# Performance work log

Measured on AMD Instinct MI355X. Metric: run time of the kernel, lower is better.

The kernel has to match this reference:

```python
import jax, jax.numpy as jnp
import numpy as np

C = 256
CQK = C // 8  # 32

def setup_inputs() -> dict:
    key = jax.random.key(0)
    ks = jax.random.split(key, 8)
    B, H, W = 8, 64, 64
    x = jax.random.normal(ks[0], (B, C, H, W), dtype=jnp.float32)
    y = jax.random.normal(ks[1], (B, C, H, W), dtype=jnp.float32)
    s = 1.0 / np.sqrt(C)
    Wq = jax.random.normal(ks[2], (CQK, C), dtype=jnp.float32) * s
    bq = jnp.zeros((CQK,), dtype=jnp.float32)
    Wk = jax.random.normal(ks[3], (CQK, C), dtype=jnp.float32) * s
    bk = jnp.zeros((CQK,), dtype=jnp.float32)
    Wv = jax.random.normal(ks[4], (C, C), dtype=jnp.float32) * s
    bv = jnp.zeros((C,), dtype=jnp.float32)
    return {"x": x, "y": y, "Wq": Wq, "bq": bq, "Wk": Wk, "bk": bk, "Wv": Wv, "bv": bv}

def reference(x, y, Wq, bq, Wk, bk, Wv, bv):
    B, Cc, H, W = x.shape
    HW = H * W
    xf = x.reshape(B, Cc, HW)  # [B,C,HW]
    yf = y.reshape(B, Cc, HW)
    # 1x1 convs == per-pixel linear projections
    Q = jnp.einsum('oc,bcn->bno', Wq, xf) + bq          # [B,HW,CQK]
    K = jnp.einsum('oc,bcn->bon', Wk, yf) + bk[:, None]  # [B,CQK,HW]
    V = jnp.einsum('oc,bcn->bon', Wv, yf) + bv[:, None]  # [B,C,HW]
    attn = jax.nn.softmax(jnp.einsum('bnd,bdm->bnm', Q, K), axis=-1)  # [B,HW,HW]
    out = jnp.einsum('bcm,bnm->bcn', V, attn)  # V @ attn^T -> [B,C,HW]
    return out.reshape(B, Cc, H, W)
```

## Files before the change

kernel.cpp:

```cpp
#include <hip/hip_runtime.h>

typedef unsigned short u16;
typedef _Float16 f16;
typedef __attribute__((ext_vector_type(8))) short v8s;
typedef __attribute__((ext_vector_type(4))) short v4s;
typedef __attribute__((ext_vector_type(8))) f16   v8h;
typedef __attribute__((ext_vector_type(4))) float v4f;
typedef __attribute__((ext_vector_type(16))) float v16f;
typedef __attribute__((ext_vector_type(4))) unsigned v4u;

#define NB   8
#define NC   256
#define DQK  32
#define NPIX 4096

__device__ __forceinline__ u16 f2bf(float f) {
  unsigned u = __builtin_bit_cast(unsigned, f);
  u += 0x7FFFu + ((u >> 16) & 1u);
  return (u16)(u >> 16);
}
__device__ __forceinline__ u16 f2h(float f) {
  return __builtin_bit_cast(u16, (f16)f);
}
__device__ __forceinline__ unsigned cvt_pk_bf16(float lo, float hi) {
  unsigned r;
  asm("v_cvt_pk_bf16_f32 %0, %1, %2" : "=v"(r) : "v"(lo), "v"(hi));
  return r;
}
__device__ __forceinline__ float fast_exp2(float x) {
  float r;
  asm("v_exp_f32 %0, %1" : "=v"(r) : "v"(x));
  return r;
}

__global__ __launch_bounds__(256)
void convert_w(const float* __restrict__ Wq, const float* __restrict__ Wk,
               const float* __restrict__ Wv,
               u16* __restrict__ Whq, u16* __restrict__ Whk, u16* __restrict__ Whv) {
  int i = blockIdx.x * 256 + threadIdx.x;
  if (i < 8192)       Whq[i]         = f2h(Wq[i]);
  else if (i < 16384) Whk[i - 8192]  = f2h(Wk[i - 8192]);
  else                Whv[i - 16384] = f2h(Wv[i - 16384]);
}

__global__ __launch_bounds__(256)
void proj_fused(const float* __restrict__ x, const float* __restrict__ y,
                const u16* __restrict__ Whq, const float* __restrict__ bq,
                const u16* __restrict__ Whk, const float* __restrict__ bk,
                const u16* __restrict__ Whv, const float* __restrict__ bv,
                u16* __restrict__ Qb, u16* __restrict__ Kb, u16* __restrict__ Vt) {
  __shared__ u16 Tx[64][66], Ty[64][66];

  const int tid = threadIdx.x, w = tid >> 6, lane = tid & 63;
  const int lr = lane & 15, quad = lane >> 4;
  const int nl = lane;
  const int b = blockIdx.x & 7;
  const int n0 = (blockIdx.x >> 3) * 64;
  const int n = n0 + w * 16 + lr;
  const size_t bn = ((size_t)b << 12) + n;
  const int col = w * 16 + lr;

  v4f aq[2], ak[2], av[16];
#pragma unroll
  for (int ot = 0; ot < 2; ++ot) { aq[ot] = (v4f){0.f,0.f,0.f,0.f}; ak[ot] = (v4f){0.f,0.f,0.f,0.f}; }
#pragma unroll
  for (int vt = 0; vt < 16; ++vt) av[vt] = (v4f){0.f,0.f,0.f,0.f};

#pragma unroll 1
  for (int cs = 0; cs < 4; ++cs) {
    if (cs) __syncthreads();
    const float* __restrict__ xs = x + ((size_t)b << 20) + (size_t)(cs * 64) * NPIX + n0;
    const float* __restrict__ ys = y + ((size_t)b << 20) + (size_t)(cs * 64) * NPIX + n0;
#pragma unroll
    for (int i = 0; i < 16; ++i) {
      int c = w * 16 + i;
      Tx[c][nl] = f2h(xs[(size_t)c * NPIX + nl]);
      Ty[c][nl] = f2h(ys[(size_t)c * NPIX + nl]);
    }
    __syncthreads();

    v8s tx0, tx1, ty0, ty1;
#pragma unroll
    for (int j = 0; j < 8; ++j) {
      tx0[j] = (short)Tx[quad * 8 + j][col];
      tx1[j] = (short)Tx[32 + quad * 8 + j][col];
      ty0[j] = (short)Ty[quad * 8 + j][col];
      ty1[j] = (short)Ty[32 + quad * 8 + j][col];
    }
    const v8h xb0 = __builtin_bit_cast(v8h, tx0);
    const v8h xb1 = __builtin_bit_cast(v8h, tx1);
    const v8h yb0 = __builtin_bit_cast(v8h, ty0);
    const v8h yb1 = __builtin_bit_cast(v8h, ty1);

#pragma unroll
    for (int ot = 0; ot < 2; ++ot) {
      const u16* wqp = Whq + (ot * 16 + lr) * 256 + cs * 64 + quad * 8;
      const u16* wkp = Whk + (ot * 16 + lr) * 256 + cs * 64 + quad * 8;
      aq[ot] = __builtin_amdgcn_mfma_f32_16x16x32_f16(*(const v8h*)(wqp),      xb0, aq[ot], 0, 0, 0);
      aq[ot] = __builtin_amdgcn_mfma_f32_16x16x32_f16(*(const v8h*)(wqp + 32), xb1, aq[ot], 0, 0, 0);
      ak[ot] = __builtin_amdgcn_mfma_f32_16x16x32_f16(*(const v8h*)(wkp),      yb0, ak[ot], 0, 0, 0);
      ak[ot] = __builtin_amdgcn_mfma_f32_16x16x32_f16(*(const v8h*)(wkp + 32), yb1, ak[ot], 0, 0, 0);
    }
#pragma unroll
    for (int vt = 0; vt < 16; ++vt) {
      const u16* wvp = Whv + (vt * 16 + lr) * 256 + cs * 64 + quad * 8;
      av[vt] = __builtin_amdgcn_mfma_f32_16x16x32_f16(*(const v8h*)(wvp),      yb0, av[vt], 0, 0, 0);
      av[vt] = __builtin_amdgcn_mfma_f32_16x16x32_f16(*(const v8h*)(wvp + 32), yb1, av[vt], 0, 0, 0);
    }
  }

#pragma unroll
  for (int ot = 0; ot < 2; ++ot) {
    v4f bqv = *(const v4f*)(bq + ot * 16 + quad * 4);
    v4f bkv = *(const v4f*)(bk + ot * 16 + quad * 4);
    v4s q4, k4;
#pragma unroll
    for (int r = 0; r < 4; ++r) {
      q4[r] = (short)f2h(aq[ot][r] + bqv[r]);
      k4[r] = (short)f2h(ak[ot][r] + bkv[r]);
    }
    *(v4s*)(Qb + bn * DQK + ot * 16 + quad * 4) = q4;
    *(v4s*)(Kb + bn * DQK + ot * 16 + quad * 4) = k4;
  }

#pragma unroll
  for (int vt = 0; vt < 16; ++vt) {
#pragma unroll
    for (int r = 0; r < 4; ++r) {
      int o = vt * 16 + quad * 4 + r;
      size_t off = ((((size_t)b * 64 + (n >> 6)) * 32 + (o >> 5) * 4 + ((n >> 4) & 3)) * 64
                    + ((n >> 3) & 1) * 32 + (o & 31)) * 8 + (n & 7);
      Vt[off] = f2bf(av[vt][r] + bv[o]);
    }
  }
}

#define L2E  1.44269504f
#define SHFT -48.0f

#define PACK_TILE(S, PBLO, PBHI)                                              \
  {                                                                           \
    float e0  = fast_exp2(fmaf(S[0],  L2E, SHFT));                            \
    float e1  = fast_exp2(fmaf(S[1],  L2E, SHFT));                            \
    float e2  = fast_exp2(fmaf(S[2],  L2E, SHFT));                            \
    float e3  = fast_exp2(fmaf(S[3],  L2E, SHFT));                            \
    float e4  = fast_exp2(fmaf(S[4],  L2E, SHFT));                            \
    float e5  = fast_exp2(fmaf(S[5],  L2E, SHFT));                            \
    float e6  = fast_exp2(fmaf(S[6],  L2E, SHFT));                            \
    float e7  = fast_exp2(fmaf(S[7],  L2E, SHFT));                            \
    float e8  = fast_exp2(fmaf(S[8],  L2E, SHFT));                            \
    float e9  = fast_exp2(fmaf(S[9],  L2E, SHFT));                            \
    float e10 = fast_exp2(fmaf(S[10], L2E, SHFT));                            \
    float e11 = fast_exp2(fmaf(S[11], L2E, SHFT));                            \
    float e12 = fast_exp2(fmaf(S[12], L2E, SHFT));                            \
    float e13 = fast_exp2(fmaf(S[13], L2E, SHFT));                            \
    float e14 = fast_exp2(fmaf(S[14], L2E, SHFT));                            \
    float e15 = fast_exp2(fmaf(S[15], L2E, SHFT));                            \
    lsum += (((e0 + e1) + (e2 + e3)) + ((e4 + e5) + (e6 + e7)))               \
          + (((e8 + e9) + (e10 + e11)) + ((e12 + e13) + (e14 + e15)));        \
    unsigned u00 = cvt_pk_bf16(e0,  e1),  u01 = cvt_pk_bf16(e2,  e3);         \
    unsigned u10 = cvt_pk_bf16(e4,  e5),  u11 = cvt_pk_bf16(e6,  e7);         \
    unsigned u20 = cvt_pk_bf16(e8,  e9),  u21 = cvt_pk_bf16(e10, e11);        \
    unsigned u30 = cvt_pk_bf16(e12, e13), u31 = cvt_pk_bf16(e14, e15);        \
    asm("v_permlane32_swap_b32 %0, %1" : "+v"(u00), "+v"(u10));               \
    asm("v_permlane32_swap_b32 %0, %1" : "+v"(u01), "+v"(u11));               \
    asm("v_permlane32_swap_b32 %0, %1" : "+v"(u20), "+v"(u30));               \
    asm("v_permlane32_swap_b32 %0, %1" : "+v"(u21), "+v"(u31));               \
    PBLO = __builtin_bit_cast(v8s, (v4u){u00, u01, u10, u11});                \
    PBHI = __builtin_bit_cast(v8s, (v4u){u20, u21, u30, u31});                \
  }

__global__ __launch_bounds__(512, 2)
void attn_kernel(const u16* __restrict__ Qb, const u16* __restrict__ Kb,
                 const u16* __restrict__ Vt, float* __restrict__ out) {
  __shared__ __attribute__((aligned(16))) u16 Vb[4][32][64][8];
  __shared__ float Ls2[4][32];

  const int tid  = threadIdx.x;
  const int w    = tid >> 6;
  const int lane = tid & 63;
  const int l31  = lane & 31;
  const int wq   = w & 3;
  const int g    = w >> 2;
  const int bufbase = g * 2;

  const int b  = blockIdx.x & 7;
  const int q0 = (blockIdx.x >> 3) << 7;
  const int qw = q0 + wq * 32;

  const int h = lane >> 5;
  const u16* Qp = Qb + ((size_t)b * NPIX + qw + l31) * DQK + h * 8;
  const v8h qf0 = *(const v8h*)(Qp);
  const v8h qf1 = *(const v8h*)(Qp + 16);

  const u16* Kp = Kb + ((size_t)b * NPIX + l31) * DQK + h * 8 + (size_t)g * 32 * 2048;

  const u16* Vg = Vt + ((size_t)b << 20) + (size_t)lane * 8 + (size_t)g * 32 * 16384;

  v16f acc[8];
#pragma unroll
  for (int i = 0; i < 8; ++i) acc[i] = (v16f){};
  float lsum = 0.f;
  const v16f vz = (v16f){};

#pragma unroll
  for (int j = 0; j < 8; ++j) {
    const int f = wq * 8 + j;
    __builtin_amdgcn_global_load_lds(
        (const __attribute__((address_space(1))) unsigned*)(Vg + (size_t)f * 512),
        (__attribute__((address_space(3))) unsigned*)(&Vb[bufbase][f][0][0]), 16, 0, 0);
  }
  v8h kc0 = *(const v8h*)(Kp);
  v8h kc1 = *(const v8h*)(Kp + 16);
  v8h kc2 = *(const v8h*)(Kp + 1024);
  v8h kc3 = *(const v8h*)(Kp + 1040);
  v8h kn0 = kc0, kn1 = kc1, kn2 = kc2, kn3 = kc3;

  v8s pB0, pB1, pB2, pB3;
  {
    v16f sA = __builtin_amdgcn_mfma_f32_32x32x16_f16(kc0, qf0, vz, 0, 0, 0);
    sA = __builtin_amdgcn_mfma_f32_32x32x16_f16(kc1, qf1, sA, 0, 0, 0);
    v16f sB = __builtin_amdgcn_mfma_f32_32x32x16_f16(kc2, qf0, vz, 0, 0, 0);
    sB = __builtin_amdgcn_mfma_f32_32x32x16_f16(kc3, qf1, sB, 0, 0, 0);
    PACK_TILE(sA, pB0, pB1);
    PACK_TILE(sB, pB2, pB3);
  }
  {
    const u16* kp1 = Kp + 2048;
    kc0 = *(const v8h*)(kp1);
    kc1 = *(const v8h*)(kp1 + 16);
    kc2 = *(const v8h*)(kp1 + 1024);
    kc3 = *(const v8h*)(kp1 + 1040);
  }

#pragma unroll 1
  for (int it = 0; it < 32; ++it) {
    const int pp = it & 1;
    __builtin_amdgcn_sched_barrier(0);
    if (it < 31) {
      asm volatile("s_waitcnt vmcnt(4)" ::: "memory");
    } else {
      asm volatile("s_waitcnt vmcnt(0)" ::: "memory");
    }
    __builtin_amdgcn_s_barrier();
    __builtin_amdgcn_sched_barrier(0);

    if (it < 31) {
#pragma unroll
      for (int j = 0; j < 8; ++j) {
        const int f = wq * 8 + j;
        __builtin_amdgcn_global_load_lds(
            (const __attribute__((address_space(1))) unsigned*)(Vg + ((size_t)(it + 1) * 32 + f) * 512),
            (__attribute__((address_space(3))) unsigned*)(&Vb[bufbase + (pp ^ 1)][f][0][0]), 16, 0, 0);
      }
    }

    __builtin_amdgcn_s_setprio(1);
#pragma unroll
    for (int ct = 0; ct < 8; ++ct) {
      v8s vf0 = *(const v8s*)(&Vb[bufbase + pp][ct * 4 + 0][lane][0]);
      v8s vf1 = *(const v8s*)(&Vb[bufbase + pp][ct * 4 + 1][lane][0]);
      v8s vf2 = *(const v8s*)(&Vb[bufbase + pp][ct * 4 + 2][lane][0]);
      v8s vf3 = *(const v8s*)(&Vb[bufbase + pp][ct * 4 + 3][lane][0]);
      acc[ct] = __builtin_amdgcn_mfma_f32_32x32x16_bf16(vf0, pB0, acc[ct], 0, 0, 0);
      acc[ct] = __builtin_amdgcn_mfma_f32_32x32x16_bf16(vf1, pB1, acc[ct], 0, 0, 0);
      acc[ct] = __builtin_amdgcn_mfma_f32_32x32x16_bf16(vf2, pB2, acc[ct], 0, 0, 0);
      acc[ct] = __builtin_amdgcn_mfma_f32_32x32x16_bf16(vf3, pB3, acc[ct], 0, 0, 0);
    }
    __builtin_amdgcn_s_setprio(0);

    if (it < 31) {
      v16f sA = __builtin_amdgcn_mfma_f32_32x32x16_f16(kc0, qf0, vz, 0, 0, 0);
      sA = __builtin_amdgcn_mfma_f32_32x32x16_f16(kc1, qf1, sA, 0, 0, 0);
      v16f sB = __builtin_amdgcn_mfma_f32_32x32x16_f16(kc2, qf0, vz, 0, 0, 0);
      sB = __builtin_amdgcn_mfma_f32_32x32x16_f16(kc3, qf1, sB, 0, 0, 0);
      if (it < 30) {
        const u16* kp2 = Kp + (size_t)(it + 2) * 2048;
        kn0 = *(const v8h*)(kp2);
        kn1 = *(const v8h*)(kp2 + 16);
        kn2 = *(const v8h*)(kp2 + 1024);
        kn3 = *(const v8h*)(kp2 + 1040);
      }
      PACK_TILE(sA, pB0, pB1);
      PACK_TILE(sB, pB2, pB3);
      kc0 = kn0; kc1 = kn1; kc2 = kn2; kc3 = kn3;
    }
  }

  lsum += __shfl_xor(lsum, 32);

  __syncthreads();
  float* Cb = (float*)&Vb[0][0][0][0];
  if (w >= 4) {
    const int w4 = w - 4;
#pragma unroll
    for (int ct = 0; ct < 8; ++ct)
#pragma unroll
      for (int k = 0; k < 4; ++k) {
        v4f c = {acc[ct][k * 4 + 0], acc[ct][k * 4 + 1],
                 acc[ct][k * 4 + 2], acc[ct][k * 4 + 3]};
        *(v4f*)(Cb + (((w4 * 32 + ct * 4 + k) * 64 + lane) << 2)) = c;
      }
    if (lane < 32) Ls2[w4][l31] = lsum;
  }
  __syncthreads();
  if (w < 4) {
    const float linv = 1.0f / (lsum + Ls2[w][l31]);
#pragma unroll
    for (int ct = 0; ct < 8; ++ct)
#pragma unroll
      for (int k = 0; k < 4; ++k) {
        v4f c = *(const v4f*)(Cb + (((w * 32 + ct * 4 + k) * 64 + lane) << 2));
        acc[ct][k * 4 + 0] += c[0]; acc[ct][k * 4 + 1] += c[1];
        acc[ct][k * 4 + 2] += c[2]; acc[ct][k * 4 + 3] += c[3];
      }

    float* op = out + (size_t)b * NC * NPIX + q0 + wq * 32 + l31;
#pragma unroll
    for (int ct = 0; ct < 8; ++ct)
#pragma unroll
      for (int r = 0; r < 16; ++r) {
        const int ch = ct * 32 + (r & 3) + ((r >> 2) << 3) + (h << 2);
        op[(size_t)ch * NPIX] = acc[ct][r] * linv;
      }
  }
}

extern "C" void kernel_launch(void* const* d_in, const int* in_sizes, int n_in,
                              void* d_out, int out_size, void* d_ws, size_t ws_size,
                              hipStream_t stream) {
  const float* x  = (const float*)d_in[0];
  const float* y  = (const float*)d_in[1];
  const float* Wq = (const float*)d_in[2];
  const float* bq = (const float*)d_in[3];
  const float* Wk = (const float*)d_in[4];
  const float* bk = (const float*)d_in[5];
  const float* Wv = (const float*)d_in[6];
  const float* bv = (const float*)d_in[7];
  float* out = (float*)d_out;

  u16* Qb  = (u16*)d_ws;
  u16* Kb  = Qb + (size_t)NB * NPIX * DQK;
  u16* Vt  = Kb + (size_t)NB * NPIX * DQK;
  u16* Whq = Vt + (size_t)NB * NC * NPIX;
  u16* Whk = Whq + 32 * 256;
  u16* Whv = Whk + 32 * 256;

  hipLaunchKernelGGL(convert_w, dim3(320), dim3(256), 0, stream, Wq, Wk, Wv, Whq, Whk, Whv);
  hipLaunchKernelGGL(proj_fused, dim3(512), dim3(256), 0, stream,
                     x, y, Whq, bq, Whk, bk, Whv, bv, Qb, Kb, Vt);
  hipLaunchKernelGGL(attn_kernel, dim3(256), dim3(512), 0, stream, Qb, Kb, Vt, out);
}
```

Measured before the change: 237.0 us.

## Fuse weight conversion, projections and attention into one cooperative kernel

Merges the three kernels into one cooperative launch, with grid-wide syncs separating weight conversion, the Q/K/V projection and attention. This removes two launch gaps. The projection now handles 128 pixels per 512-thread block, register-prefetches the next channel slab and writes the transposed tile to LDS with vector stores. The attention loop is unrolled by two with ping-pong P registers, and the next V stage is issued right after the barrier. Grid syncs add cost and require all 256 blocks to be co-resident.

```diff
diff --git a/kernel.cpp b/kernel.cpp
--- a/kernel.cpp
+++ b/kernel.cpp
@@ -1,4 +1,7 @@
 #include <hip/hip_runtime.h>
+#include <hip/hip_cooperative_groups.h>
+
+namespace cg = cooperative_groups;
 
 typedef unsigned short u16;
 typedef _Float16 f16;
@@ -31,108 +34,6 @@
   float r;
   asm("v_exp_f32 %0, %1" : "=v"(r) : "v"(x));
   return r;
-}
-
-__global__ __launch_bounds__(256)
-void convert_w(const float* __restrict__ Wq, const float* __restrict__ Wk,
-               const float* __restrict__ Wv,
-               u16* __restrict__ Whq, u16* __restrict__ Whk, u16* __restrict__ Whv) {
-  int i = blockIdx.x * 256 + threadIdx.x;
-  if (i < 8192)       Whq[i]         = f2h(Wq[i]);
-  else if (i < 16384) Whk[i - 8192]  = f2h(Wk[i - 8192]);
-  else                Whv[i - 16384] = f2h(Wv[i - 16384]);
-}
-
-__global__ __launch_bounds__(256)
-void proj_fused(const float* __restrict__ x, const float* __restrict__ y,
-                const u16* __restrict__ Whq, const float* __restrict__ bq,
-                const u16* __restrict__ Whk, const float* __restrict__ bk,
-                const u16* __restrict__ Whv, const float* __restrict__ bv,
-                u16* __restrict__ Qb, u16* __restrict__ Kb, u16* __restrict__ Vt) {
-  __shared__ u16 Tx[64][66], Ty[64][66];
-
-  const int tid = threadIdx.x, w = tid >> 6, lane = tid & 63;
-  const int lr = lane & 15, quad = lane >> 4;
-  const int nl = lane;
-  const int b = blockIdx.x & 7;
-  const int n0 = (blockIdx.x >> 3) * 64;
-  const int n = n0 + w * 16 + lr;
-  const size_t bn = ((size_t)b << 12) + n;
-  const int col = w * 16 + lr;
-
-  v4f aq[2], ak[2], av[16];
-#pragma unroll
-  for (int ot = 0; ot < 2; ++ot) { aq[ot] = (v4f){0.f,0.f,0.f,0.f}; ak[ot] = (v4f){0.f,0.f,0.f,0.f}; }
-#pragma unroll
-  for (int vt = 0; vt < 16; ++vt) av[vt] = (v4f){0.f,0.f,0.f,0.f};
-
-#pragma unroll 1
-  for (int cs = 0; cs < 4; ++cs) {
-    if (cs) __syncthreads();
-    const float* __restrict__ xs = x + ((size_t)b << 20) + (size_t)(cs * 64) * NPIX + n0;
-    const float* __restrict__ ys = y + ((size_t)b << 20) + (size_t)(cs * 64) * NPIX + n0;
-#pragma unroll
-    for (int i = 0; i < 16; ++i) {
-      int c = w * 16 + i;
-      Tx[c][nl] = f2h(xs[(size_t)c * NPIX + nl]);
-      Ty[c][nl] = f2h(ys[(size_t)c * NPIX + nl]);
-    }
-    __syncthreads();
-
-    v8s tx0, tx1, ty0, ty1;
-#pragma unroll
-    for (int j = 0; j < 8; ++j) {
-      tx0[j] = (short)Tx[quad * 8 + j][col];
-      tx1[j] = (short)Tx[32 + quad * 8 + j][col];
-      ty0[j] = (short)Ty[quad * 8 + j][col];
-      ty1[j] = (short)Ty[32 + quad * 8 + j][col];
-    }
-    const v8h xb0 = __builtin_bit_cast(v8h, tx0);
-    const v8h xb1 = __builtin_bit_cast(v8h, tx1);
-    const v8h yb0 = __builtin_bit_cast(v8h, ty0);
-    const v8h yb1 = __builtin_bit_cast(v8h, ty1);
-
-#pragma unroll
-    for (int ot = 0; ot < 2; ++ot) {
-      const u16* wqp = Whq + (ot * 16 + lr) * 256 + cs * 64 + quad * 8;
-      const u16* wkp = Whk + (ot * 16 + lr) * 256 + cs * 64 + quad * 8;
-      aq[ot] = __builtin_amdgcn_mfma_f32_16x16x32_f16(*(const v8h*)(wqp),      xb0, aq[ot], 0, 0, 0);
-      aq[ot] = __builtin_amdgcn_mfma_f32_16x16x32_f16(*(const v8h*)(wqp + 32), xb1, aq[ot], 0, 0, 0);
-      ak[ot] = __builtin_amdgcn_mfma_f32_16x16x32_f16(*(const v8h*)(wkp),      yb0, ak[ot], 0, 0, 0);
-      ak[ot] = __builtin_amdgcn_mfma_f32_16x16x32_f16(*(const v8h*)(wkp + 32), yb1, ak[ot], 0, 0, 0);
-    }
-#pragma unroll
-    for (int vt = 0; vt < 16; ++vt) {
-      const u16* wvp = Whv + (vt * 16 + lr) * 256 + cs * 64 + quad * 8;
-      av[vt] = __builtin_amdgcn_mfma_f32_16x16x32_f16(*(const v8h*)(wvp),      yb0, av[vt], 0, 0, 0);
-      av[vt] = __builtin_amdgcn_mfma_f32_16x16x32_f16(*(const v8h*)(wvp + 32), yb1, av[vt], 0, 0, 0);
-    }
-  }
-
-#pragma unroll
-  for (int ot = 0; ot < 2; ++ot) {
-    v4f bqv = *(const v4f*)(bq + ot * 16 + quad * 4);
-    v4f bkv = *(const v4f*)(bk + ot * 16 + quad * 4);
-    v4s q4, k4;
-#pragma unroll
-    for (int r = 0; r < 4; ++r) {
-      q4[r] = (short)f2h(aq[ot][r] + bqv[r]);
-      k4[r] = (short)f2h(ak[ot][r] + bkv[r]);
-    }
-    *(v4s*)(Qb + bn * DQK + ot * 16 + quad * 4) = q4;
-    *(v4s*)(Kb + bn * DQK + ot * 16 + quad * 4) = k4;
-  }
-
-#pragma unroll
-  for (int vt = 0; vt < 16; ++vt) {
-#pragma unroll
-    for (int r = 0; r < 4; ++r) {
-      int o = vt * 16 + quad * 4 + r;
-      size_t off = ((((size_t)b * 64 + (n >> 6)) * 32 + (o >> 5) * 4 + ((n >> 4) & 3)) * 64
-                    + ((n >> 3) & 1) * 32 + (o & 31)) * 8 + (n & 7);
-      Vt[off] = f2bf(av[vt][r] + bv[o]);
-    }
-  }
 }
 
 #define L2E  1.44269504f
@@ -170,159 +71,263 @@
     PBHI = __builtin_bit_cast(v8s, (v4u){u20, u21, u30, u31});                \
   }
 
+#define STAGE(IT, BUF)                                                        \
+  {                                                                           \
+    _Pragma("unroll")                                                         \
+    for (int j = 0; j < 8; ++j) {                                             \
+      const int f = wq * 8 + j;                                               \
+      __builtin_amdgcn_global_load_lds(                                       \
+          (const __attribute__((address_space(1))) unsigned*)(Vg + ((size_t)(IT) * 32 + f) * 512), \
+          (__attribute__((address_space(3))) unsigned*)(&SB[BUF][f][0][0]), 16, 0, 0); \
+    }                                                                         \
+  }
+
+#define ASTEP(I, PP, PI0, PI1, PI2, PI3, PO0, PO1, PO2, PO3)                  \
+  {                                                                           \
+    __builtin_amdgcn_sched_barrier(0);                                        \
+    if ((I) < 31) { asm volatile("s_waitcnt vmcnt(4)" ::: "memory"); }        \
+    else          { asm volatile("s_waitcnt vmcnt(0)" ::: "memory"); }        \
+    __builtin_amdgcn_s_barrier();                                             \
+    __builtin_amdgcn_sched_barrier(0);                                        \
+    if ((I) < 31) {                                                           \
+      STAGE((I) + 1, bufbase + ((PP) ^ 1));                                   \
+      v16f sA = __builtin_amdgcn_mfma_f32_32x32x16_f16(kc0, qf0, vz, 0, 0, 0);\
+      sA = __builtin_amdgcn_mfma_f32_32x32x16_f16(kc1, qf1, sA, 0, 0, 0);     \
+      PACK_TILE(sA, PO0, PO1);                                                \
+      v16f sB = __builtin_amdgcn_mfma_f32_32x32x16_f16(kc2, qf0, vz, 0, 0, 0);\
+      sB = __builtin_amdgcn_mfma_f32_32x32x16_f16(kc3, qf1, sB, 0, 0, 0);     \
+      PACK_TILE(sB, PO2, PO3);                                                \
+    }                                                                         \
+    if ((I) < 30) {   \
+      const u16* kp2 = Kp + (size_t)((I) + 2) * 2048;                         \
+      kc0 = *(const v8h*)(kp2);                                               \
+      kc1 = *(const v8h*)(kp2 + 16);                                          \
+      kc2 = *(const v8h*)(kp2 + 1024);                                        \
+      kc3 = *(const v8h*)(kp2 + 1040);                                        \
+    }                                                                         \
+    __builtin_amdgcn_s_setprio(1);                                            \
+    _Pragma("unroll")                                                         \
+    for (int ct = 0; ct < 8; ++ct) {                                          \
+      v8s vf0 = *(const v8s*)(&SB[bufbase + (PP)][ct * 4 + 0][lane][0]);      \
+      v8s vf1 = *(const v8s*)(&SB[bufbase + (PP)][ct * 4 + 1][lane][0]);      \
+      v8s vf2 = *(const v8s*)(&SB[bufbase + (PP)][ct * 4 + 2][lane][0]);      \
+      v8s vf3 = *(const v8s*)(&SB[bufbase + (PP)][ct * 4 + 3][lane][0]);      \
+      acc[ct] = __builtin_amdgcn_mfma_f32_32x32x16_bf16(vf0, PI0, acc[ct], 0, 0, 0); \
+      acc[ct] = __builtin_amdgcn_mfma_f32_32x32x16_bf16(vf1, PI1, acc[ct], 0, 0, 0); \
+      acc[ct] = __builtin_amdgcn_mfma_f32_32x32x16_bf16(vf2, PI2, acc[ct], 0, 0, 0); \
+      acc[ct] = __builtin_amdgcn_mfma_f32_32x32x16_bf16(vf3, PI3, acc[ct], 0, 0, 0); \
+    }                                                                         \
+    __builtin_amdgcn_s_setprio(0);                                            \
+  }
+
 __global__ __launch_bounds__(512, 2)
-void attn_kernel(const u16* __restrict__ Qb, const u16* __restrict__ Kb,
-                 const u16* __restrict__ Vt, float* __restrict__ out) {
-  __shared__ __attribute__((aligned(16))) u16 Vb[4][32][64][8];
+void fused_all(const float* __restrict__ x, const float* __restrict__ y,
+               const float* __restrict__ Wq, const float* __restrict__ bq,
+               const float* __restrict__ Wk, const float* __restrict__ bk,
+               const float* __restrict__ Wv, const float* __restrict__ bv,
+               u16* __restrict__ Qb, u16* __restrict__ Kb, u16* __restrict__ Vt,
+               u16* __restrict__ Whq, u16* __restrict__ Whk, u16* __restrict__ Whv,
+               float* __restrict__ out) {
+  __shared__ __attribute__((aligned(16))) u16 SB[4][32][64][8];
   __shared__ float Ls2[4][32];
 
   const int tid  = threadIdx.x;
   const int w    = tid >> 6;
   const int lane = tid & 63;
-  const int l31  = lane & 31;
-  const int wq   = w & 3;
-  const int g    = w >> 2;
-  const int bufbase = g * 2;
-
-  const int b  = blockIdx.x & 7;
-  const int q0 = (blockIdx.x >> 3) << 7;
-  const int qw = q0 + wq * 32;
-
-  const int h = lane >> 5;
-  const u16* Qp = Qb + ((size_t)b * NPIX + qw + l31) * DQK + h * 8;
-  const v8h qf0 = *(const v8h*)(Qp);
-  const v8h qf1 = *(const v8h*)(Qp + 16);
-
-  const u16* Kp = Kb + ((size_t)b * NPIX + l31) * DQK + h * 8 + (size_t)g * 32 * 2048;
-
-  const u16* Vg = Vt + ((size_t)b << 20) + (size_t)lane * 8 + (size_t)g * 32 * 16384;
-
-  v16f acc[8];
-#pragma unroll
-  for (int i = 0; i < 8; ++i) acc[i] = (v16f){};
-  float lsum = 0.f;
-  const v16f vz = (v16f){};
-
-#pragma unroll
-  for (int j = 0; j < 8; ++j) {
-    const int f = wq * 8 + j;
-    __builtin_amdgcn_global_load_lds(
-        (const __attribute__((address_space(1))) unsigned*)(Vg + (size_t)f * 512),
-        (__attribute__((address_space(3))) unsigned*)(&Vb[bufbase][f][0][0]), 16, 0, 0);
-  }
-  v8h kc0 = *(const v8h*)(Kp);
-  v8h kc1 = *(const v8h*)(Kp + 16);
-  v8h kc2 = *(const v8h*)(Kp + 1024);
-  v8h kc3 = *(const v8h*)(Kp + 1040);
-  v8h kn0 = kc0, kn1 = kc1, kn2 = kc2, kn3 = kc3;
-
-  v8s pB0, pB1, pB2, pB3;
+  const int lr   = lane & 15;
+  const int quad = lane >> 4;
+  const int b    = blockIdx.x & 7;
+  const int n0   = (blockIdx.x >> 3) * 128;
+
   {
-    v16f sA = __builtin_amdgcn_mfma_f32_32x32x16_f16(kc0, qf0, vz, 0, 0, 0);
-    sA = __builtin_amdgcn_mfma_f32_32x32x16_f16(kc1, qf1, sA, 0, 0, 0);
-    v16f sB = __builtin_amdgcn_mfma_f32_32x32x16_f16(kc2, qf0, vz, 0, 0, 0);
-    sB = __builtin_amdgcn_mfma_f32_32x32x16_f16(kc3, qf1, sB, 0, 0, 0);
-    PACK_TILE(sA, pB0, pB1);
-    PACK_TILE(sB, pB2, pB3);
-  }
+    int i = blockIdx.x * 512 + tid;
+    if (i < 8192)       Whq[i]         = f2h(Wq[i]);
+    else if (i < 16384) Whk[i - 8192]  = f2h(Wk[i - 8192]);
+    else if (i < 81920) Whv[i - 16384] = f2h(Wv[i - 16384]);
+  }
+  __threadfence();
+  cg::this_grid().sync();
+
   {
-    const u16* kp1 = Kp + 2048;
-    kc0 = *(const v8h*)(kp1);
-    kc1 = *(const v8h*)(kp1 + 16);
-    kc2 = *(const v8h*)(kp1 + 1024);
-    kc3 = *(const v8h*)(kp1 + 1040);
-  }
+    u16 (*Tx)[88] = reinterpret_cast<u16 (*)[88]>(&SB[0][0][0][0]);
+    u16 (*Ty)[88] = Tx + 128;
+
+    const int col = w * 16 + lr;
+    const int n = n0 + col;
+    const size_t bn = ((size_t)b << 12) + n;
+    const int srow  = (w >> 2) * 64 + lane;
+    const int scol0 = (w & 3) * 16;
+    const float* __restrict__ xs = x + ((size_t)b << 20) + n0 + srow;
+    const float* __restrict__ ys = y + ((size_t)b << 20) + n0 + srow;
+
+    v4f aq[2], ak[2], av[16];
+#pragma unroll
+    for (int ot = 0; ot < 2; ++ot) { aq[ot] = (v4f){0.f,0.f,0.f,0.f}; ak[ot] = (v4f){0.f,0.f,0.f,0.f}; }
+#pragma unroll
+    for (int vt = 0; vt < 16; ++vt) av[vt] = (v4f){0.f,0.f,0.f,0.f};
+
+    float xv[16], yv[16];
+#pragma unroll
+    for (int i = 0; i < 16; ++i) {
+      xv[i] = xs[(size_t)(scol0 + i) * NPIX];
+      yv[i] = ys[(size_t)(scol0 + i) * NPIX];
+    }
 
 #pragma unroll 1
-  for (int it = 0; it < 32; ++it) {
-    const int pp = it & 1;
-    __builtin_amdgcn_sched_barrier(0);
-    if (it < 31) {
-      asm volatile("s_waitcnt vmcnt(4)" ::: "memory");
-    } else {
-      asm volatile("s_waitcnt vmcnt(0)" ::: "memory");
-    }
-    __builtin_amdgcn_s_barrier();
-    __builtin_amdgcn_sched_barrier(0);
-
-    if (it < 31) {
-#pragma unroll
-      for (int j = 0; j < 8; ++j) {
-        const int f = wq * 8 + j;
-        __builtin_amdgcn_global_load_lds(
-            (const __attribute__((address_space(1))) unsigned*)(Vg + ((size_t)(it + 1) * 32 + f) * 512),
-            (__attribute__((address_space(3))) unsigned*)(&Vb[bufbase + (pp ^ 1)][f][0][0]), 16, 0, 0);
-      }
-    }
-
-    __builtin_amdgcn_s_setprio(1);
-#pragma unroll
-    for (int ct = 0; ct < 8; ++ct) {
-      v8s vf0 = *(const v8s*)(&Vb[bufbase + pp][ct * 4 + 0][lane][0]);
-      v8s vf1 = *(const v8s*)(&Vb[bufbase + pp][ct * 4 + 1][lane][0]);
-      v8s vf2 = *(const v8s*)(&Vb[bufbase + pp][ct * 4 + 2][lane][0]);
-      v8s vf3 = *(const v8s*)(&Vb[bufbase + pp][ct * 4 + 3][lane][0]);
-      acc[ct] = __builtin_amdgcn_mfma_f32_32x32x16_bf16(vf0, pB0, acc[ct], 0, 0, 0);
-      acc[ct] = __builtin_amdgcn_mfma_f32_32x32x16_bf16(vf1, pB1, acc[ct], 0, 0, 0);
-      acc[ct] = __builtin_amdgcn_mfma_f32_32x32x16_bf16(vf2, pB2, acc[ct], 0, 0, 0);
-      acc[ct] = __builtin_amdgcn_mfma_f32_32x32x16_bf16(vf3, pB3, acc[ct], 0, 0, 0);
-    }
-    __builtin_amdgcn_s_setprio(0);
-
-    if (it < 31) {
-      v16f sA = __builtin_amdgcn_mfma_f32_32x32x16_f16(kc0, qf0, vz, 0, 0, 0);
-      sA = __builtin_amdgcn_mfma_f32_32x32x16_f16(kc1, qf1, sA, 0, 0, 0);
-      v16f sB = __builtin_amdgcn_mfma_f32_32x32x16_f16(kc2, qf0, vz, 0, 0, 0);
-      sB = __builtin_amdgcn_mfma_f32_32x32x16_f16(kc3, qf1, sB, 0, 0, 0);
-      if (it < 30) {
-        const u16* kp2 = Kp + (size_t)(it + 2) * 2048;
-        kn0 = *(const v8h*)(kp2);
-        kn1 = *(const v8h*)(kp2 + 16);
-        kn2 = *(const v8h*)(kp2 + 1024);
-        kn3 = *(const v8h*)(kp2 + 1040);
-      }
-      PACK_TILE(sA, pB0, pB1);
-      PACK_TILE(sB, pB2, pB3);
-      kc0 = kn0; kc1 = kn1; kc2 = kn2; kc3 = kn3;
-    }
-  }
-
-  lsum += __shfl_xor(lsum, 32);
-
-  __syncthreads();
-  float* Cb = (float*)&Vb[0][0][0][0];
-  if (w >= 4) {
-    const int w4 = w - 4;
-#pragma unroll
-    for (int ct = 0; ct < 8; ++ct)
-#pragma unroll
-      for (int k = 0; k < 4; ++k) {
-        v4f c = {acc[ct][k * 4 + 0], acc[ct][k * 4 + 1],
-                 acc[ct][k * 4 + 2], acc[ct][k * 4 + 3]};
-        *(v4f*)(Cb + (((w4 * 32 + ct * 4 + k) * 64 + lane) << 2)) = c;
-      }
-    if (lane < 32) Ls2[w4][l31] = lsum;
-  }
-  __syncthreads();
-  if (w < 4) {
-    const float linv = 1.0f / (lsum + Ls2[w][l31]);
-#pragma unroll
-    for (int ct = 0; ct < 8; ++ct)
-#pragma unroll
-      for (int k = 0; k < 4; ++k) {
-        v4f c = *(const v4f*)(Cb + (((w * 32 + ct * 4 + k) * 64 + lane) << 2));
-        acc[ct][k * 4 + 0] += c[0]; acc[ct][k * 4 + 1] += c[1];
-        acc[ct][k * 4 + 2] += c[2]; acc[ct][k * 4 + 3] += c[3];
-      }
-
-    float* op = out + (size_t)b * NC * NPIX + q0 + wq * 32 + l31;
-#pragma unroll
-    for (int ct = 0; ct < 8; ++ct)
-#pragma unroll
-      for (int r = 0; r < 16; ++r) {
-        const int ch = ct * 32 + (r & 3) + ((r >> 2) << 3) + (h << 2);
-        op[(size_t)ch * NPIX] = acc[ct][r] * linv;
-      }
+    for (int cs = 0; cs < 4; ++cs) {
+      __syncthreads();
+      v8s hx0, hx1, hy0, hy1;
+#pragma unroll
+      for (int i = 0; i < 8; ++i) {
+        hx0[i] = (short)f2h(xv[i]);     hx1[i] = (short)f2h(xv[8 + i]);
+        hy0[i] = (short)f2h(yv[i]);     hy1[i] = (short)f2h(yv[8 + i]);
+      }
+      *(v8s*)(&Tx[srow][scol0])     = hx0;
+      *(v8s*)(&Tx[srow][scol0 + 8]) = hx1;
+      *(v8s*)(&Ty[srow][scol0])     = hy0;
+      *(v8s*)(&Ty[srow][scol0 + 8]) = hy1;
+      if (cs < 3) {
+#pragma unroll
+        for (int i = 0; i < 16; ++i) {
+          xv[i] = xs[(size_t)((cs + 1) * 64 + scol0 + i) * NPIX];
+          yv[i] = ys[(size_t)((cs + 1) * 64 + scol0 + i) * NPIX];
+        }
+      }
+      __syncthreads();
+
+      const v8h xb0 = *(const v8h*)(&Tx[col][quad * 8]);
+      const v8h xb1 = *(const v8h*)(&Tx[col][32 + quad * 8]);
+      const v8h yb0 = *(const v8h*)(&Ty[col][quad * 8]);
+      const v8h yb1 = *(const v8h*)(&Ty[col][32 + quad * 8]);
+
+#pragma unroll
+      for (int ot = 0; ot < 2; ++ot) {
+        const u16* wqp = Whq + (ot * 16 + lr) * 256 + cs * 64 + quad * 8;
+        const u16* wkp = Whk + (ot * 16 + lr) * 256 + cs * 64 + quad * 8;
+        aq[ot] = __builtin_amdgcn_mfma_f32_16x16x32_f16(*(const v8h*)(wqp),      xb0, aq[ot], 0, 0, 0);
+        aq[ot] = __builtin_amdgcn_mfma_f32_16x16x32_f16(*(const v8h*)(wqp + 32), xb1, aq[ot], 0, 0, 0);
+        ak[ot] = __builtin_amdgcn_mfma_f32_16x16x32_f16(*(const v8h*)(wkp),      yb0, ak[ot], 0, 0, 0);
+        ak[ot] = __builtin_amdgcn_mfma_f32_16x16x32_f16(*(const v8h*)(wkp + 32), yb1, ak[ot], 0, 0, 0);
+      }
+#pragma unroll
+      for (int vt = 0; vt < 16; ++vt) {
+        const u16* wvp = Whv + (vt * 16 + lr) * 256 + cs * 64 + quad * 8;
+        av[vt] = __builtin_amdgcn_mfma_f32_16x16x32_f16(*(const v8h*)(wvp),      yb0, av[vt], 0, 0, 0);
+        av[vt] = __builtin_amdgcn_mfma_f32_16x16x32_f16(*(const v8h*)(wvp + 32), yb1, av[vt], 0, 0, 0);
+      }
+    }
+
+#pragma unroll
+    for (int ot = 0; ot < 2; ++ot) {
+      v4f bqv = *(const v4f*)(bq + ot * 16 + quad * 4);
+      v4f bkv = *(const v4f*)(bk + ot * 16 + quad * 4);
+      v4s q4, k4;
+#pragma unroll
+      for (int r = 0; r < 4; ++r) {
+        q4[r] = (short)f2h(aq[ot][r] + bqv[r]);
+        k4[r] = (short)f2h(ak[ot][r] + bkv[r]);
+      }
+      *(v4s*)(Qb + bn * DQK + ot * 16 + quad * 4) = q4;
+      *(v4s*)(Kb + bn * DQK + ot * 16 + quad * 4) = k4;
+    }
+#pragma unroll
+    for (int vt = 0; vt < 16; ++vt) {
+#pragma unroll
+      for (int r = 0; r < 4; ++r) {
+        int o = vt * 16 + quad * 4 + r;
+        size_t off = ((((size_t)b * 64 + (n >> 6)) * 32 + (o >> 5) * 4 + ((n >> 4) & 3)) * 64
+                      + ((n >> 3) & 1) * 32 + (o & 31)) * 8 + (n & 7);
+        Vt[off] = f2bf(av[vt][r] + bv[o]);
+      }
+    }
+  }
+  __threadfence();
+  cg::this_grid().sync();
+
+  {
+    const int l31 = lane & 31;
+    const int h   = lane >> 5;
+    const int wq  = w & 3;
+    const int g   = w >> 2;
+    const int bufbase = g * 2;
+    const int q0 = n0;
+    const int qw = q0 + wq * 32;
+
+    const u16* Qp = Qb + ((size_t)b * NPIX + qw + l31) * DQK + h * 8;
+    const v8h qf0 = *(const v8h*)(Qp);
+    const v8h qf1 = *(const v8h*)(Qp + 16);
+    const u16* Kp = Kb + ((size_t)b * NPIX + l31) * DQK + h * 8 + (size_t)g * 32 * 2048;
+    const u16* Vg = Vt + ((size_t)b << 20) + (size_t)lane * 8 + (size_t)g * 32 * 16384;
+
+    v16f acc[8];
+#pragma unroll
+    for (int i = 0; i < 8; ++i) acc[i] = (v16f){};
+    float lsum = 0.f;
+    const v16f vz = (v16f){};
+
+    v8h kc0, kc1, kc2, kc3;
+    v8s pA0, pA1, pA2, pA3, pB0, pB1, pB2, pB3;
+    STAGE(0, bufbase);
+    {
+      v8h t0 = *(const v8h*)(Kp);
+      v8h t1 = *(const v8h*)(Kp + 16);
+      v8h t2 = *(const v8h*)(Kp + 1024);
+      v8h t3 = *(const v8h*)(Kp + 1040);
+      v16f sA = __builtin_amdgcn_mfma_f32_32x32x16_f16(t0, qf0, vz, 0, 0, 0);
+      sA = __builtin_amdgcn_mfma_f32_32x32x16_f16(t1, qf1, sA, 0, 0, 0);
+      PACK_TILE(sA, pA0, pA1);
+      v16f sB = __builtin_amdgcn_mfma_f32_32x32x16_f16(t2, qf0, vz, 0, 0, 0);
+      sB = __builtin_amdgcn_mfma_f32_32x32x16_f16(t3, qf1, sB, 0, 0, 0);
+      PACK_TILE(sB, pA2, pA3);
+      const u16* kp1 = Kp + 2048;
+      kc0 = *(const v8h*)(kp1);
+      kc1 = *(const v8h*)(kp1 + 16);
+      kc2 = *(const v8h*)(kp1 + 1024);
+      kc3 = *(const v8h*)(kp1 + 1040);
+    }
+
+#pragma unroll 1
+    for (int t = 0; t < 16; ++t) {
+      ASTEP(2 * t,     0, pA0, pA1, pA2, pA3, pB0, pB1, pB2, pB3);
+      ASTEP(2 * t + 1, 1, pB0, pB1, pB2, pB3, pA0, pA1, pA2, pA3);
+    }
+
+    lsum += __shfl_xor(lsum, 32);
+
+    __syncthreads();
+    float* Cb = (float*)&SB[0][0][0][0];
+    if (w >= 4) {
+      const int w4 = w - 4;
+#pragma unroll
+      for (int ct = 0; ct < 8; ++ct)
+#pragma unroll
+        for (int k = 0; k < 4; ++k) {
+          v4f c = {acc[ct][k * 4 + 0], acc[ct][k * 4 + 1],
+                   acc[ct][k * 4 + 2], acc[ct][k * 4 + 3]};
+          *(v4f*)(Cb + (((w4 * 32 + ct * 4 + k) * 64 + lane) << 2)) = c;
+        }
+      if (lane < 32) Ls2[w4][l31] = lsum;
+    }
+    __syncthreads();
+    if (w < 4) {
+      const float linv = 1.0f / (lsum + Ls2[w][l31]);
+#pragma unroll
+      for (int ct = 0; ct < 8; ++ct)
+#pragma unroll
+        for (int k = 0; k < 4; ++k) {
+          v4f c = *(const v4f*)(Cb + (((w * 32 + ct * 4 + k) * 64 + lane) << 2));
+          acc[ct][k * 4 + 0] += c[0]; acc[ct][k * 4 + 1] += c[1];
+          acc[ct][k * 4 + 2] += c[2]; acc[ct][k * 4 + 3] += c[3];
+        }
+      float* op = out + (size_t)b * NC * NPIX + q0 + wq * 32 + l31;
+#pragma unroll
+      for (int ct = 0; ct < 8; ++ct)
+#pragma unroll
+        for (int r = 0; r < 16; ++r) {
+          const int ch = ct * 32 + (r & 3) + ((r >> 2) << 3) + (h << 2);
+          op[(size_t)ch * NPIX] = acc[ct][r] * linv;
+        }
+    }
   }
 }
 
@@ -346,8 +351,7 @@
   u16* Whk = Whq + 32 * 256;
   u16* Whv = Whk + 32 * 256;
 
-  hipLaunchKernelGGL(convert_w, dim3(320), dim3(256), 0, stream, Wq, Wk, Wv, Whq, Whk, Whv);
-  hipLaunchKernelGGL(proj_fused, dim3(512), dim3(256), 0, stream,
-                     x, y, Whq, bq, Whk, bk, Whv, bv, Qb, Kb, Vt);
-  hipLaunchKernelGGL(attn_kernel, dim3(256), dim3(512), 0, stream, Qb, Kb, Vt, out);
-}
+  void* args[] = {&x, &y, &Wq, &bq, &Wk, &bk, &Wv, &bv,
+                  &Qb, &Kb, &Vt, &Whq, &Whk, &Whv, &out};
+  hipLaunchCooperativeKernel((void*)fused_all, dim3(256), dim3(512), args, 0, stream);
+}
```

Result: slower. 409.8 us (+72.9%).
